# Kernel tuning notes

Hardware: AMD Instinct MI355X
Metric: run time of the kernel (lower is better)

Reference implementation:

```python
import jax, jax.numpy as jnp
import numpy as np

EPS = 1e-8


def l2norm(x, axis):
    # matches torch: x / (sqrt(sum(x^2)) + eps)
    return x / (jnp.sqrt(jnp.sum(x * x, axis=axis, keepdims=True)) + EPS)


def setup_inputs() -> dict:
    key = jax.random.key(0)
    k1, k2, k3, k4, k5 = jax.random.split(key, 5)
    I, C, L, R, D = 16, 32, 32, 36, 1024  # n_image, n_caption, max_words, n_regions, embed_dim
    img_emb = l2norm(jax.random.normal(k1, (I, R, D), jnp.float32), -1)
    cap_emb = l2norm(jax.random.normal(k2, (C, L, D), jnp.float32), -1)
    W_emb = jax.random.normal(k3, (D, D), jnp.float32)  # nn.Embedding weight, N(0,1) default init
    sim_map_w = 2.5 + 0.1 * jax.random.normal(k4, (1, D), jnp.float32)  # init_weight: normal(2.5, 0.1)
    temp_scale_w = jnp.full((1, 1), np.log(1.0 / 0.07), jnp.float32)    # init_weight
    temp_learnable_w = jnp.full((1, 1), 4.0, jnp.float32)               # init_weight
    cap_lens = jax.random.randint(k5, (C,), 4, L + 1, jnp.int32)        # ragged caption lengths in [4, L]
    return dict(img_emb=img_emb, cap_emb=cap_emb, W_emb=W_emb, sim_map_w=sim_map_w,
                temp_scale_w=temp_scale_w, temp_learnable_w=temp_learnable_w, cap_lens=cap_lens)


def reference(img_emb, cap_emb, W_emb, sim_map_w, temp_scale_w, temp_learnable_w, cap_lens):
    D = W_emb.shape[0]
    L = cap_emb.shape[1]
    # --- dimension-weight branch (caption-independent) ---
    # linspace(0, D, D).long(): last index is D (out of range in torch); gather with clip.
    idx = jnp.floor(jnp.linspace(0.0, D, D)).astype(jnp.int32)
    weights = jax.nn.sigmoid(jnp.take(W_emb, idx, axis=0, mode='clip'))  # (D, D)
    mean_p = jnp.mean(weights, axis=1)                  # (D,)
    std_p = jnp.std(weights, axis=1, ddof=1)            # torch.std is unbiased
    thres = mean_p + sim_map_w[0] * std_p               # (D,)
    values = jnp.exp(temp_learnable_w[0, 0]) * (weights - thres[:, None])
    mask_p = jnp.tanh(jnp.exp(values))
    Dlw = l2norm(mask_p * weights, axis=1)              # Dim_learned_weights (D, D)
    diag = Dlw.sum(0)                                   # Diagonal (D,); diag_embed matmul == elementwise scale
    smooth = jnp.exp(temp_scale_w[0, 0])
    # --- vectorized ragged per-caption cross attention ---
    wmask = (jnp.arange(L)[None, :] < cap_lens[:, None]).astype(cap_emb.dtype)  # (C, L)
    # attn[c,i,l,r] = tanh(sum_d cap[c,l,d] * diag[d] * img[i,r,d])
    attn = jnp.tanh(jnp.einsum('cld,ird->cilr', cap_emb, img_emb * diag))
    attn = jnp.where(attn >= 0, attn, 0.1 * attn) * wmask[:, None, :, None]  # LeakyReLU(0.1), zero padded words
    attn = attn / (jnp.sqrt(jnp.sum(attn * attn, axis=2, keepdims=True)) + EPS)  # l2norm over word dim
    attn = jax.nn.softmax(attn * smooth, axis=3)        # softmax over regions
    ctx = l2norm(jnp.einsum('cilr,ird->cild', attn, img_emb), axis=-1)  # Context_img
    sim_loc = ctx * cap_emb[:, None, :, :]
    sim_sub = jnp.einsum('cild,ed->cile', sim_loc, Dlw)  # sim_loc @ Dlw.T
    sim_vec = l2norm(sim_sub, axis=-1).sum(-1)           # (C, I, L)
    # mean over the n_word valid words of each caption
    sim = jnp.sum(sim_vec * wmask[:, None, :], axis=2) / cap_lens[:, None].astype(cap_emb.dtype)  # (C, I)
    return sim.T  # (n_image, n_caption), matching torch.cat(sim_all, 1)
```

## Files before the change

kernel.cpp:

```cpp
#include <hip/hip_runtime.h>
#include <hip/hip_bf16.h>

#define I_N 16
#define C_N 32
#define L_N 32
#define R_N 36
#define D_N 1024
#define EPSF 1e-8f

typedef _Float16 f16;
typedef __attribute__((ext_vector_type(8))) _Float16 half8;
typedef __attribute__((ext_vector_type(4))) float floatx4;

__device__ __forceinline__ void gl16(const f16* g, f16* l) {
  __builtin_amdgcn_global_load_lds(
      (const __attribute__((address_space(1))) void*)g,
      (__attribute__((address_space(3))) void*)l, 16, 0, 0);
}

__device__ __forceinline__ float blk_sum_256(float v, float* red) {
  #pragma unroll
  for (int off = 32; off > 0; off >>= 1) v += __shfl_down(v, off, 64);
  int wid = threadIdx.x >> 6;
  if ((threadIdx.x & 63) == 0) red[wid] = v;
  __syncthreads();
  float s = red[0] + red[1] + red[2] + red[3];
  __syncthreads();
  return s;
}

__global__ __launch_bounds__(256) void k_dlw(const float* __restrict__ W,
    const float* __restrict__ simw, const float* __restrict__ tlw,
    float* __restrict__ Dlw, f16* __restrict__ DlwH) {
  int row = blockIdx.x, tid = threadIdx.x;
  __shared__ float red[4];
  const float* Wr = W + (size_t)row * D_N;
  float w[4]; float p = 0.f;
  #pragma unroll
  for (int k = 0; k < 4; ++k) {
    int j = tid + k * 256;
    float x = Wr[j];
    w[k] = 1.f / (1.f + expf(-x));
    p += w[k];
  }
  float S = blk_sum_256(p, red);
  float mean = S * (1.f / 1024.f);
  p = 0.f;
  #pragma unroll
  for (int k = 0; k < 4; ++k) { float d = w[k] - mean; p += d * d; }
  float S2 = blk_sum_256(p, red);
  float stdv = sqrtf(S2 * (1.f / 1023.f));
  float thres = mean + simw[row] * stdv;
  float eT = expf(tlw[0]);
  float mw[4]; p = 0.f;
  #pragma unroll
  for (int k = 0; k < 4; ++k) {
    float val = eT * (w[k] - thres);
    float mp = tanhf(expf(val));
    mw[k] = mp * w[k];
    p += mw[k] * mw[k];
  }
  float S3 = blk_sum_256(p, red);
  float inv = 1.f / (sqrtf(S3) + EPSF);
  #pragma unroll
  for (int k = 0; k < 4; ++k) {
    int j = tid + k * 256;
    float v = mw[k] * inv;
    Dlw[(size_t)row * D_N + j] = v;
    DlwH[(size_t)row * D_N + j] = (f16)v;
  }
}

__global__ __launch_bounds__(256) void k_diag_part(const float* __restrict__ Dlw,
                                                   float* __restrict__ dpart) {
  int col = blockIdx.x * 256 + threadIdx.x;
  int p = blockIdx.y;
  float s = 0.f;
  #pragma unroll 8
  for (int r = p * 64; r < p * 64 + 64; ++r) s += Dlw[(size_t)r * D_N + col];
  dpart[(size_t)p * D_N + col] = s;
}

__global__ __launch_bounds__(256) void k_diag2p(const float* __restrict__ dpart,
    const int* __restrict__ lens, float* __restrict__ diag,
    int* __restrict__ pfx, int* __restrict__ mp) {
  if (blockIdx.x < 4) {
    int col = blockIdx.x * 256 + threadIdx.x;
    float s = 0.f;
    #pragma unroll
    for (int p = 0; p < 16; ++p) s += dpart[(size_t)p * D_N + col];
    diag[col] = s;
  } else if (threadIdx.x < 64) {
    int l = threadIdx.x;
    int v = (l < 32) ? lens[l] : 0;
    int s = v;
    #pragma unroll
    for (int off = 1; off < 32; off <<= 1) {
      int t = __shfl_up(s, off, 64);
      if (l >= off) s += t;
    }
    if (l < 32) pfx[l] = s - v;
    if (l == 31) { pfx[32] = s; mp[0] = s * 16; }
  }
}

__global__ __launch_bounds__(256) void k_prep(const float* __restrict__ cap,
    const float* __restrict__ img, const float* __restrict__ diag,
    f16* __restrict__ capH, f16* __restrict__ imgH, f16* __restrict__ imgdH) {
  int bid = blockIdx.x;
  if (bid < 1024) {
    size_t base = (size_t)bid * D_N;
    #pragma unroll
    for (int k = 0; k < 4; ++k) {
      int j = threadIdx.x + k * 256;
      capH[base + j] = (f16)cap[base + j];
    }
  } else if (bid < 1600) {
    size_t base = (size_t)(bid - 1024) * D_N;
    #pragma unroll
    for (int k = 0; k < 4; ++k) {
      int j = threadIdx.x + k * 256;
      imgH[base + j] = (f16)img[base + j];
    }
  } else {
    int row = bid - 1600;
    int i = row / 48, r = row % 48;
    size_t dst = (size_t)row * D_N;
    if (r < R_N) {
      size_t src = ((size_t)i * R_N + r) * D_N;
      #pragma unroll
      for (int k = 0; k < 4; ++k) {
        int j = threadIdx.x + k * 256;
        imgdH[dst + j] = (f16)(img[src + j] * diag[j]);
      }
    } else {
      #pragma unroll
      for (int k = 0; k < 4; ++k) {
        int j = threadIdx.x + k * 256;
        imgdH[dst + j] = (f16)0.f;
      }
    }
  }
}

__global__ __launch_bounds__(256) void k_qk(const f16* __restrict__ A,
    const f16* __restrict__ B, float* __restrict__ qk) {
  int mt = blockIdx.x;
  int i  = blockIdx.y;
  int tid = threadIdx.x;
  int w = tid >> 6, lane = tid & 63;
  int l15 = lane & 15, h = lane >> 4;
  __shared__ __align__(16) f16 Als[64 * 32];
  __shared__ __align__(16) f16 Bls[48 * 32];
  floatx4 acc[3];
  #pragma unroll
  for (int nf = 0; nf < 3; ++nf) acc[nf] = (floatx4)0.f;
  int arow = tid >> 2;
  int u = tid & 3;
  int vf = (u | ((arow & 1) << 2)) ^ ((arow >> 1) & 7);
  int wofs = (((arow & 62) | (vf >> 2)) * 32) + (vf & 3) * 8;
  const f16* Ag = A + (size_t)(mt * 64 + arow) * D_N + u * 8;
  const f16* Bg = B + (size_t)(i * 48 + arow) * D_N + u * 8;
  int v2 = (h | ((l15 & 1) << 2)) ^ ((l15 >> 1) & 7);
  int rbit = (v2 >> 2) & 1;
  int pun = (v2 & 3) * 8;
  int aoff = (w * 16 + (l15 & 14) + rbit) * 32 + pun;
  int boff[3];
  #pragma unroll
  for (int nf = 0; nf < 3; ++nf) boff[nf] = (nf * 16 + (l15 & 14) + rbit) * 32 + pun;
  for (int kk = 0; kk < D_N; kk += 32) {
    *(float4*)(&Als[wofs]) = *(const float4*)(Ag + kk);
    if (tid < 192) *(float4*)(&Bls[wofs]) = *(const float4*)(Bg + kk);
    __syncthreads();
    half8 a = *(const half8*)(&Als[aoff]);
    #pragma unroll
    for (int nf = 0; nf < 3; ++nf) {
      half8 b = *(const half8*)(&Bls[boff[nf]]);
      acc[nf] = __builtin_amdgcn_mfma_f32_16x16x32_f16(a, b, acc[nf], 0, 0, 0);
    }
    __syncthreads();
  }
  #pragma unroll
  for (int nf = 0; nf < 3; ++nf)
    #pragma unroll
    for (int j = 0; j < 4; ++j) {
      int m = mt * 64 + w * 16 + h * 4 + j;
      int n = nf * 16 + l15;
      qk[(size_t)m * 768 + i * 48 + n] = acc[nf][j];
    }
}

__global__ __launch_bounds__(256) void k_attnsm(const float* __restrict__ qk,
    const int* __restrict__ lens, const float* __restrict__ tsw,
    float* __restrict__ pw) {
  int c = blockIdx.x >> 4, i = blockIdx.x & 15;
  int tid = threadIdx.x;
  int len = lens[c];
  float smooth = expf(tsw[0]);
  __shared__ float att[L_N][R_N];
  __shared__ float cn[R_N];
  for (int e = tid; e < L_N * R_N; e += 256) {
    int l = e / R_N, r = e % R_N;
    float x = qk[(size_t)(c * 32 + l) * 768 + i * 48 + r];
    float t = tanhf(x);
    float v = (t >= 0.f) ? t : 0.1f * t;
    if (l >= len) v = 0.f;
    att[l][r] = v;
  }
  __syncthreads();
  if (tid < R_N) {
    float s = 0.f;
    #pragma unroll
    for (int l = 0; l < L_N; ++l) s += att[l][tid] * att[l][tid];
    cn[tid] = sqrtf(s) + EPSF;
  }
  __syncthreads();
  if (tid < L_N) {
    float z[R_N];
    float mx = -3.4e38f;
    #pragma unroll
    for (int r = 0; r < R_N; ++r) { z[r] = att[tid][r] / cn[r] * smooth; mx = fmaxf(mx, z[r]); }
    float se = 0.f;
    #pragma unroll
    for (int r = 0; r < R_N; ++r) { float e = expf(z[r] - mx); z[r] = e; se += e; }
    float inv = 1.f / se;
    #pragma unroll
    for (int r = 0; r < R_N; ++r) att[tid][r] = z[r] * inv;
  }
  __syncthreads();
  for (int e = tid; e < L_N * R_N; e += 256) {
    int l = e / R_N, r = e % R_N;
    pw[((size_t)i * 1024 + c * 32 + l) * R_N + r] = att[l][r];
  }
}

__global__ __launch_bounds__(256) void k_ctx(const float* __restrict__ pw,
    const f16* __restrict__ imgH, const float* __restrict__ cap,
    const int* __restrict__ lens, const int* __restrict__ pfx,
    f16* __restrict__ slc) {
  int c  = blockIdx.x;
  int i  = blockIdx.y;
  int tid = threadIdx.x;
  int w = tid >> 6;
  int cg = tid & 63;
  int len = lens[c];
  int pf = pfx[c];
  __shared__ float pA[32][R_N];
  __shared__ __align__(16) f16 rows[R_N][1024];
  for (int e = tid; e < 32 * R_N; e += 256) {
    int rr = e / R_N, r = e % R_N;
    pA[rr][r] = pw[((size_t)i * 1024 + c * 32 + rr) * R_N + r];
  }
  const f16* base = imgH + (size_t)i * R_N * D_N;
  #pragma unroll
  for (int t = 0; t < 9; ++t) {
    int rr = w * 9 + t;
    const f16* src = base + (size_t)rr * D_N + cg * 8;
    gl16(src,       &rows[rr][0]);
    gl16(src + 512, &rows[rr][512]);
  }
  __syncthreads();
  int d0 = cg * 8, d1 = 512 + cg * 8;
  #pragma unroll
  for (int sub = 0; sub < 2; ++sub) {
    float acc[4][16];
    #pragma unroll
    for (int j = 0; j < 4; ++j)
      #pragma unroll
      for (int q = 0; q < 16; ++q) acc[j][q] = 0.f;
    for (int k = 0; k < R_N; ++k) {
      half8 h0 = *(const half8*)(&rows[k][d0]);
      half8 h1 = *(const half8*)(&rows[k][d1]);
      float bv[16];
      #pragma unroll
      for (int q = 0; q < 8; ++q) { bv[q] = (float)h0[q]; bv[8 + q] = (float)h1[q]; }
      #pragma unroll
      for (int j = 0; j < 4; ++j) {
        float a = pA[sub * 16 + w * 4 + j][k];
        #pragma unroll
        for (int q = 0; q < 16; ++q) acc[j][q] += a * bv[q];
      }
    }
    #pragma unroll
    for (int j = 0; j < 4; ++j) {
      int l = sub * 16 + w * 4 + j;
      float ss = 0.f;
      #pragma unroll
      for (int q = 0; q < 16; ++q) ss += acc[j][q] * acc[j][q];
      #pragma unroll
      for (int off = 1; off < 64; off <<= 1) ss += __shfl_xor(ss, off, 64);
      if (l < len) {
        float inv = 1.f / (sqrtf(ss) + EPSF);
        const float* capr = cap + ((size_t)c * L_N + l) * D_N;
        float4 c0 = *(const float4*)(capr + d0);
        float4 c1 = *(const float4*)(capr + d0 + 4);
        float4 c2 = *(const float4*)(capr + d1);
        float4 c3 = *(const float4*)(capr + d1 + 4);
        float cv[16] = {c0.x,c0.y,c0.z,c0.w, c1.x,c1.y,c1.z,c1.w,
                        c2.x,c2.y,c2.z,c2.w, c3.x,c3.y,c3.z,c3.w};
        union { f16 h[16]; float4 f4[2]; } u;
        #pragma unroll
        for (int q = 0; q < 16; ++q) u.h[q] = (f16)(acc[j][q] * inv * cv[q]);
        f16* dst = slc + ((size_t)((pf + l) * 16 + i)) * D_N;
        *(float4*)(dst + d0) = u.f4[0];
        *(float4*)(dst + d1) = u.f4[1];
      }
    }
  }
}

__global__ __launch_bounds__(256) void k_gemm(const f16* __restrict__ A,
    const f16* __restrict__ B, const int* __restrict__ mp,
    float* __restrict__ rs16, float* __restrict__ rq16) {
  int bx = blockIdx.x, by = blockIdx.y;
  int Mp = mp[0];
  int m0 = bx * 128, n0 = by * 128;
  if (m0 >= Mp) return;
  int tid = threadIdx.x;
  int w = tid >> 6, lane = tid & 63;
  int l15 = lane & 15, h = lane >> 4;
  int wm = w >> 1, wn = w & 1;
  __shared__ __align__(16) f16 AB[3][2][128 * 32];
  floatx4 acc[4][4];
  #pragma unroll
  for (int mf = 0; mf < 4; ++mf)
    #pragma unroll
    for (int nf = 0; nf < 4; ++nf) acc[mf][nf] = (floatx4)0.f;

  int r_p = lane >> 2, u_p = lane & 3;
  int sw = (r_p >> 1) & 7;
  int val = (u_p | ((r_p & 1) << 2)) ^ sw;
  int r_l = (r_p & 14) | (val >> 2);
  int u_l = val & 3;
  const f16* As0 = A + (size_t)(m0 + w * 32 +  0 + r_l) * D_N + u_l * 8;
  const f16* As1 = A + (size_t)(m0 + w * 32 + 16 + r_l) * D_N + u_l * 8;
  const f16* Bs0 = B + (size_t)(n0 + w * 32 +  0 + r_l) * D_N + u_l * 8;
  const f16* Bs1 = B + (size_t)(n0 + w * 32 + 16 + r_l) * D_N + u_l * 8;

  int v2 = (h | ((l15 & 1) << 2)) ^ ((l15 >> 1) & 7);
  int rbit = (v2 >> 2) & 1;
  int pun = (v2 & 3) * 8;
  int aoff[4], boff[4];
  #pragma unroll
  for (int f = 0; f < 4; ++f) {
    aoff[f] = (wm * 64 + f * 16 + (l15 & 14) + rbit) * 32 + pun;
    boff[f] = (wn * 64 + f * 16 + (l15 & 14) + rbit) * 32 + pun;
  }

  #define STAGE(kt, b) { \
    int kof = (kt) * 32; \
    gl16(As0 + kof, &AB[b][0][(w * 32 +  0) * 32]); \
    gl16(As1 + kof, &AB[b][0][(w * 32 + 16) * 32]); \
    gl16(Bs0 + kof, &AB[b][1][(w * 32 +  0) * 32]); \
    gl16(Bs1 + kof, &AB[b][1][(w * 32 + 16) * 32]); }

  #define COMPUTE(b) { \
    half8 af[4], bf[4]; \
    _Pragma("unroll") for (int f = 0; f < 4; ++f) af[f] = *(const half8*)(&AB[b][0][aoff[f]]); \
    _Pragma("unroll") for (int f = 0; f < 4; ++f) bf[f] = *(const half8*)(&AB[b][1][boff[f]]); \
    _Pragma("unroll") for (int mf = 0; mf < 4; ++mf) \
      _Pragma("unroll") for (int nf = 0; nf < 4; ++nf) \
        acc[mf][nf] = __builtin_amdgcn_mfma_f32_16x16x32_f16(af[mf], bf[nf], acc[mf][nf], 0, 0, 0); }

  STAGE(0, 0);
  STAGE(1, 1);
  int cur = 0, n2 = 2;
  for (int kk = 0; kk < 30; ++kk) {
    STAGE(kk + 2, n2);
    asm volatile("s_waitcnt vmcnt(8)" ::: "memory");
    __builtin_amdgcn_s_barrier();
    __builtin_amdgcn_sched_barrier(0);
    COMPUTE(cur);
    __builtin_amdgcn_s_barrier();
    cur = (cur == 2) ? 0 : cur + 1;
    n2  = (n2  == 2) ? 0 : n2  + 1;
  }
  asm volatile("s_waitcnt vmcnt(4)" ::: "memory");
  __builtin_amdgcn_s_barrier();
  __builtin_amdgcn_sched_barrier(0);
  COMPUTE(cur);
  __builtin_amdgcn_s_barrier();
  cur = (cur == 2) ? 0 : cur + 1;
  asm volatile("s_waitcnt vmcnt(0)" ::: "memory");
  __builtin_amdgcn_s_barrier();
  __builtin_amdgcn_sched_barrier(0);
  COMPUTE(cur);
  #undef STAGE
  #undef COMPUTE

  int slot = by * 2 + wn;
  #pragma unroll
  for (int mf = 0; mf < 4; ++mf)
    #pragma unroll
    for (int j = 0; j < 4; ++j) {
      float s = 0.f, q = 0.f;
      #pragma unroll
      for (int nf = 0; nf < 4; ++nf) { float v = acc[mf][nf][j]; s += v; q += v * v; }
      #pragma unroll
      for (int off = 1; off < 16; off <<= 1) { s += __shfl_xor(s, off, 64); q += __shfl_xor(q, off, 64); }
      if (l15 == 0) {
        int m = m0 + wm * 64 + mf * 16 + h * 4 + j;
        rs16[(size_t)slot * 16384 + m] = s;
        rq16[(size_t)slot * 16384 + m] = q;
      }
    }
}

__global__ __launch_bounds__(64) void k_final(const float* __restrict__ rs16,
    const float* __restrict__ rq16, const int* __restrict__ lens,
    const int* __restrict__ pfx, float* __restrict__ out) {
  int b = blockIdx.x;
  int c = b & 31;
  int l = threadIdx.x;
  int len = lens[c];
  float sv = 0.f;
  if (l < len) {
    int i = b >> 5;
    int row = (pfx[c] + l) * 16 + i;
    float rs = 0.f, rq = 0.f;
    #pragma unroll
    for (int s = 0; s < 16; ++s) {
      rs += rs16[(size_t)s * 16384 + row];
      rq += rq16[(size_t)s * 16384 + row];
    }
    sv = rs / (sqrtf(rq) + EPSF);
  }
  #pragma unroll
  for (int off = 32; off > 0; off >>= 1) sv += __shfl_down(sv, off, 64);
  if (l == 0) out[b] = sv / (float)len;
}

extern "C" void kernel_launch(void* const* d_in, const int* in_sizes, int n_in,
                              void* d_out, int out_size, void* d_ws, size_t ws_size,
                              hipStream_t stream) {
  const float* img  = (const float*)d_in[0];
  const float* cap  = (const float*)d_in[1];
  const float* W    = (const float*)d_in[2];
  const float* simw = (const float*)d_in[3];
  const float* tsw  = (const float*)d_in[4];
  const float* tlw  = (const float*)d_in[5];
  const int*   lens = (const int*)d_in[6];
  float* out = (float*)d_out;

  char* wsB = (char*)d_ws;
  if (ws_size < 51122176) return;
  float* Dlw   = (float*)(wsB + 0);
  f16*   DlwH  = (f16*)  (wsB + 4194304);
  float* diag  = (float*)(wsB + 6291456);
  f16*   capH  = (f16*)  (wsB + 6295552);
  f16*   imgdH = (f16*)  (wsB + 8392704);
  float* qk    = (float*)(wsB + 9965568);
  float* pw    = (float*)(wsB + 13111296);
  f16*   slc   = (f16*)  (wsB + 15470592);
  float* rs16  = (float*)(wsB + 49025024);
  float* rq16  = (float*)(wsB + 50073600);
  float* dpart = qk;
  f16*   imgH  = (f16*)Dlw;
  int*   mp    = (int*)(wsB + 2097152);
  int*   pfx   = (int*)(wsB + 2097152 + 256);

  k_dlw<<<1024, 256, 0, stream>>>(W, simw, tlw, Dlw, DlwH);
  k_diag_part<<<dim3(4, 16), 256, 0, stream>>>(Dlw, dpart);
  k_diag2p<<<5, 256, 0, stream>>>(dpart, lens, diag, pfx, mp);
  k_prep<<<2368, 256, 0, stream>>>(cap, img, diag, capH, imgH, imgdH);
  k_qk<<<dim3(16, 16), 256, 0, stream>>>(capH, imgdH, qk);
  k_attnsm<<<512, 256, 0, stream>>>(qk, lens, tsw, pw);
  k_ctx<<<dim3(32, 16), 256, 0, stream>>>(pw, imgH, cap, lens, pfx, slc);
  k_gemm<<<dim3(128, 8), 256, 0, stream>>>(slc, DlwH, mp, rs16, rq16);
  k_final<<<512, 64, 0, stream>>>(rs16, rq16, lens, pfx, out);
}
```

Before: 106.8 us.

## Fuse attention tanh/leaky/l2norm/softmax into QK GEMM epilogue; use fast exp/tanh

Moves the attention post-processing (tanh, LeakyReLU, masking, word-dim l2norm and region softmax) into the epilogue of the QK MFMA kernel and stages the tile in shared memory. This removes one kernel launch and the global round trip of the qk intermediate. It also replaces expf/tanhf with __expf-based fast approximations in k_dlw and the attention path, which trades some accuracy for cheaper math. The softmax is now done by only 64 threads per block, which serialises the epilogue somewhat.

```diff
diff --git a/kernel.cpp b/kernel.cpp
--- a/kernel.cpp
+++ b/kernel.cpp
@@ -16,6 +16,12 @@
   __builtin_amdgcn_global_load_lds(
       (const __attribute__((address_space(1))) void*)g,
       (__attribute__((address_space(3))) void*)l, 16, 0, 0);
+}
+
+__device__ __forceinline__ float fast_tanh(float x) {
+  float q = __expf(-2.f * fabsf(x));
+  float t = (1.f - q) / (1.f + q);
+  return (x >= 0.f) ? t : -t;
 }
 
 __device__ __forceinline__ float blk_sum_256(float v, float* red) {
@@ -40,7 +46,7 @@
   for (int k = 0; k < 4; ++k) {
     int j = tid + k * 256;
     float x = Wr[j];
-    w[k] = 1.f / (1.f + expf(-x));
+    w[k] = 1.f / (1.f + __expf(-x));
     p += w[k];
   }
   float S = blk_sum_256(p, red);
@@ -51,12 +57,14 @@
   float S2 = blk_sum_256(p, red);
   float stdv = sqrtf(S2 * (1.f / 1023.f));
   float thres = mean + simw[row] * stdv;
-  float eT = expf(tlw[0]);
+  float eT = __expf(tlw[0]);
   float mw[4]; p = 0.f;
   #pragma unroll
   for (int k = 0; k < 4; ++k) {
     float val = eT * (w[k] - thres);
-    float mp = tanhf(expf(val));
+    float y = __expf(val);
+    float q = __expf(-2.f * y);
+    float mp = (1.f - q) / (1.f + q);
     mw[k] = mp * w[k];
     p += mw[k] * mw[k];
   }
@@ -144,7 +152,8 @@
 }
 
 __global__ __launch_bounds__(256) void k_qk(const f16* __restrict__ A,
-    const f16* __restrict__ B, float* __restrict__ qk) {
+    const f16* __restrict__ B, const int* __restrict__ lens,
+    const float* __restrict__ tsw, float* __restrict__ pw) {
   int mt = blockIdx.x;
   int i  = blockIdx.y;
   int tid = threadIdx.x;
@@ -152,6 +161,8 @@
   int l15 = lane & 15, h = lane >> 4;
   __shared__ __align__(16) f16 Als[64 * 32];
   __shared__ __align__(16) f16 Bls[48 * 32];
+  __shared__ float att[64][49];
+  __shared__ float cn[2][R_N];
   floatx4 acc[3];
   #pragma unroll
   for (int nf = 0; nf < 3; ++nf) acc[nf] = (floatx4)0.f;
@@ -180,57 +191,49 @@
     }
     __syncthreads();
   }
+  int len0 = lens[mt * 2], len1 = lens[mt * 2 + 1];
   #pragma unroll
   for (int nf = 0; nf < 3; ++nf)
     #pragma unroll
     for (int j = 0; j < 4; ++j) {
-      int m = mt * 64 + w * 16 + h * 4 + j;
+      int ml = w * 16 + h * 4 + j;
       int n = nf * 16 + l15;
-      qk[(size_t)m * 768 + i * 48 + n] = acc[nf][j];
-    }
-}
-
-__global__ __launch_bounds__(256) void k_attnsm(const float* __restrict__ qk,
-    const int* __restrict__ lens, const float* __restrict__ tsw,
-    float* __restrict__ pw) {
-  int c = blockIdx.x >> 4, i = blockIdx.x & 15;
-  int tid = threadIdx.x;
-  int len = lens[c];
-  float smooth = expf(tsw[0]);
-  __shared__ float att[L_N][R_N];
-  __shared__ float cn[R_N];
-  for (int e = tid; e < L_N * R_N; e += 256) {
-    int l = e / R_N, r = e % R_N;
-    float x = qk[(size_t)(c * 32 + l) * 768 + i * 48 + r];
-    float t = tanhf(x);
-    float v = (t >= 0.f) ? t : 0.1f * t;
-    if (l >= len) v = 0.f;
-    att[l][r] = v;
-  }
+      float t = fast_tanh(acc[nf][j]);
+      float v = (t >= 0.f) ? t : 0.1f * t;
+      int len = (ml >= 32) ? len1 : len0;
+      if ((ml & 31) >= len || n >= R_N) v = 0.f;
+      att[ml][n] = v;
+    }
   __syncthreads();
-  if (tid < R_N) {
+  for (int e = tid; e < 2 * R_N; e += 256) {
+    int cc = e / R_N, r = e % R_N;
     float s = 0.f;
     #pragma unroll
-    for (int l = 0; l < L_N; ++l) s += att[l][tid] * att[l][tid];
-    cn[tid] = sqrtf(s) + EPSF;
+    for (int l = 0; l < 32; ++l) { float a = att[cc * 32 + l][r]; s += a * a; }
+    cn[cc][r] = sqrtf(s) + EPSF;
   }
   __syncthreads();
-  if (tid < L_N) {
-    float z[R_N];
+  if (tid < 64) {
+    int cc = tid >> 5, l = tid & 31;
+    float smooth = __expf(tsw[0]);
     float mx = -3.4e38f;
     #pragma unroll
-    for (int r = 0; r < R_N; ++r) { z[r] = att[tid][r] / cn[r] * smooth; mx = fmaxf(mx, z[r]); }
+    for (int r = 0; r < R_N; ++r) {
+      float z = att[tid][r] / cn[cc][r] * smooth;
+      att[tid][r] = z;
+      mx = fmaxf(mx, z);
+    }
     float se = 0.f;
     #pragma unroll
-    for (int r = 0; r < R_N; ++r) { float e = expf(z[r] - mx); z[r] = e; se += e; }
+    for (int r = 0; r < R_N; ++r) {
+      float e2 = __expf(att[tid][r] - mx);
+      att[tid][r] = e2;
+      se += e2;
+    }
     float inv = 1.f / se;
-    #pragma unroll
-    for (int r = 0; r < R_N; ++r) att[tid][r] = z[r] * inv;
-  }
-  __syncthreads();
-  for (int e = tid; e < L_N * R_N; e += 256) {
-    int l = e / R_N, r = e % R_N;
-    pw[((size_t)i * 1024 + c * 32 + l) * R_N + r] = att[l][r];
+    float* dst = pw + ((size_t)i * 1024 + (mt * 2 + cc) * 32 + l) * R_N;
+    #pragma unroll
+    for (int r = 0; r < R_N; ++r) dst[r] = att[tid][r] * inv;
   }
 }
 
@@ -449,12 +452,11 @@
   float* diag  = (float*)(wsB + 6291456);
   f16*   capH  = (f16*)  (wsB + 6295552);
   f16*   imgdH = (f16*)  (wsB + 8392704);
-  float* qk    = (float*)(wsB + 9965568);
+  float* dpart = (float*)(wsB + 9965568);
   float* pw    = (float*)(wsB + 13111296);
   f16*   slc   = (f16*)  (wsB + 15470592);
   float* rs16  = (float*)(wsB + 49025024);
   float* rq16  = (float*)(wsB + 50073600);
-  float* dpart = qk;
   f16*   imgH  = (f16*)Dlw;
   int*   mp    = (int*)(wsB + 2097152);
   int*   pfx   = (int*)(wsB + 2097152 + 256);
@@ -463,8 +465,7 @@
   k_diag_part<<<dim3(4, 16), 256, 0, stream>>>(Dlw, dpart);
   k_diag2p<<<5, 256, 0, stream>>>(dpart, lens, diag, pfx, mp);
   k_prep<<<2368, 256, 0, stream>>>(cap, img, diag, capH, imgH, imgdH);
-  k_qk<<<dim3(16, 16), 256, 0, stream>>>(capH, imgdH, qk);
-  k_attnsm<<<512, 256, 0, stream>>>(qk, lens, tsw, pw);
+  k_qk<<<dim3(16, 16), 256, 0, stream>>>(capH, imgdH, lens, tsw, pw);
   k_ctx<<<dim3(32, 16), 256, 0, stream>>>(pw, imgH, cap, lens, pfx, slc);
   k_gemm<<<dim3(128, 8), 256, 0, stream>>>(slc, DlwH, mp, rs16, rq16);
   k_final<<<512, 64, 0, stream>>>(rs16, rq16, lens, pfx, out);
```

New measurement: 103.5 us. 3.1% less time.
